# Kernel tuning notes

Measured on AMD Instinct MI355X. Metric: run time of the kernel, lower is better.

## Reference

```python
import jax, jax.numpy as jnp
import numpy as np

B, T, C = 64, 4096, 256
H = 4
HD = C // H  # head_dim = 64
EPS = 1e-5   # torch LayerNorm default


def setup_inputs() -> dict:
    key = jax.random.key(0)
    ks = jax.random.split(key, 8)
    x = jax.random.normal(ks[0], (B, T, C), dtype=jnp.float32)
    # per-head score MLP: Linear(C->HD) + Tanh + Linear(HD->1, no bias)
    W1 = jax.random.normal(ks[1], (H, C, HD), dtype=jnp.float32) * (1.0 / np.sqrt(C))
    b1 = jax.random.normal(ks[2], (H, HD), dtype=jnp.float32) * 0.02
    w2 = jax.random.normal(ks[3], (H, HD), dtype=jnp.float32) * (1.0 / np.sqrt(HD))
    # output projection Linear(H*C -> C), torch layout (out, in)
    Wo = jax.random.normal(ks[4], (C, H * C), dtype=jnp.float32) * (1.0 / np.sqrt(H * C))
    bo = jax.random.normal(ks[5], (C,), dtype=jnp.float32) * 0.02
    gamma = jnp.ones((C,), dtype=jnp.float32)
    beta = jnp.zeros((C,), dtype=jnp.float32)
    return {"x": x, "W1": W1, "b1": b1, "w2": w2, "Wo": Wo, "bo": bo,
            "gamma": gamma, "beta": beta}


def reference(x, W1, b1, w2, Wo, bo, gamma, beta):
    # All heads batched: hidden (B,H,T,HD)
    h = jnp.tanh(jnp.einsum('btc,hcd->bhtd', x, W1) + b1[None, :, None, :])
    scores = jnp.einsum('bhtd,hd->bht', h, w2)            # (B,H,T)
    weights = jax.nn.softmax(scores, axis=-1)             # softmax over T
    contexts = jnp.einsum('bht,btc->bhc', weights, x)     # (B,H,C)
    multi = contexts.reshape(B, H * C)                    # concat over heads
    out = multi @ Wo.T + bo                               # Linear(H*C->C)
    # LayerNorm over last dim (dropout is identity in eval mode)
    mu = jnp.mean(out, axis=-1, keepdims=True)
    var = jnp.mean(jnp.square(out - mu), axis=-1, keepdims=True)
    out = (out - mu) * jax.lax.rsqrt(var + EPS) * gamma + beta
    return out, weights
```

## Files before the change

kernel.cpp:

```cpp
#include <hip/hip_runtime.h>
#include <hip/hip_bf16.h>
#include <math.h>

#define B_ 64
#define T_ 4096
#define C_ 256
#define H_ 4
#define HD_ 64
#define EPS_ 1e-5f

typedef __attribute__((ext_vector_type(4))) float floatx4;
typedef __attribute__((ext_vector_type(8))) short short8;

#if __has_builtin(__builtin_amdgcn_cvt_pk_bf16_f32)
typedef __attribute__((ext_vector_type(2))) __bf16 bf16x2_t;
__device__ __forceinline__ unsigned int pack_bf16x2(float a, float b) {
    bf16x2_t v = __builtin_amdgcn_cvt_pk_bf16_f32(a, b);
    return __builtin_bit_cast(unsigned int, v);
}
#else
__device__ __forceinline__ unsigned int pack_bf16x2(float a, float b) {
    unsigned int ua = __builtin_bit_cast(unsigned int, a);
    unsigned int ub = __builtin_bit_cast(unsigned int, b);
    ua = (ua + 0x7fffu + ((ua >> 16) & 1u)) >> 16;
    ub = (ub + 0x7fffu + ((ub >> 16) & 1u)) >> 16;
    return ua | (ub << 16);
}
#endif

__device__ __forceinline__ float fast_tanh(float v) {
    float a = fabsf(v);
    float e = __expf(-2.0f * a);
    float r = (1.0f - e) / (1.0f + e);
    return copysignf(r, v);
}

__global__ void k0_w1t(const float* __restrict__ W1, unsigned short* __restrict__ w1t) {
    int n = blockIdx.x;
    int c = threadIdx.x;
    int h = n >> 6, d = n & 63;
    float v = W1[(h * C_ + c) * HD_ + d];
    unsigned int u = __builtin_bit_cast(unsigned int, v);
    u = (u + 0x7fffu + ((u >> 16) & 1u)) >> 16;
    w1t[n * C_ + c] = (unsigned short)u;
}

#define ASTRIDE 264
__global__ __launch_bounds__(256, 4)
void k1_fused(const float* __restrict__ x, const unsigned short* __restrict__ w1t,
              const float* __restrict__ b1, const float* __restrict__ w2,
              float* __restrict__ rawscore, float* __restrict__ ctxp,
              float* __restrict__ mS) {
    __shared__ __align__(16) unsigned short shA[64 * ASTRIDE];
    __shared__ float sS[4 * 64];
    __shared__ __align__(16) float sP4[64 * 4];

    const int tid  = threadIdx.x;
    const int lane = tid & 63;
    const int w    = tid >> 6;
    const int nl   = lane & 15;
    const int q    = lane >> 4;
    const int rowbase = blockIdx.x * 64;
    const int b       = blockIdx.x >> 6;
    const int tbase   = (blockIdx.x & 63) * 64;

    const int arow = tid >> 2;
    const int acol = (tid & 3) * 8;
    const float* aptr = x + (long)(rowbase + arow) * C_ + acol;
    #pragma unroll
    for (int kc = 0; kc < 8; ++kc) {
        const float4* ap = (const float4*)(aptr + kc * 32);
        float4 f0 = ap[0], f1 = ap[1];
        uint4 ua;
        ua.x = pack_bf16x2(f0.x, f0.y); ua.y = pack_bf16x2(f0.z, f0.w);
        ua.z = pack_bf16x2(f1.x, f1.y); ua.w = pack_bf16x2(f1.z, f1.w);
        *(uint4*)&shA[arow * ASTRIDE + kc * 32 + acol] = ua;
    }

    floatx4 acc[4][4];
    #pragma unroll
    for (int i = 0; i < 4; ++i)
        #pragma unroll
        for (int j = 0; j < 4; ++j)
            acc[i][j] = (floatx4){0.f, 0.f, 0.f, 0.f};

    const unsigned short* bBase = w1t + (long)(w * 64 + nl) * C_ + q * 8;
    __syncthreads();

    for (int ks = 0; ks < 8; ++ks) {
        uint4 bF[4];
        #pragma unroll
        for (int nb = 0; nb < 4; ++nb)
            bF[nb] = *(const uint4*)(bBase + nb * 16 * C_ + ks * 32);
        short8 aF[4];
        #pragma unroll
        for (int mb = 0; mb < 4; ++mb)
            aF[mb] = *(const short8*)&shA[(mb * 16 + nl) * ASTRIDE + ks * 32 + q * 8];
        #pragma unroll
        for (int mb = 0; mb < 4; ++mb)
            #pragma unroll
            for (int nb = 0; nb < 4; ++nb)
                acc[mb][nb] = __builtin_amdgcn_mfma_f32_16x16x32_bf16(
                    aF[mb], __builtin_bit_cast(short8, bF[nb]), acc[mb][nb], 0, 0, 0);
    }

    float b1v[4], w2v[4];
    #pragma unroll
    for (int nb = 0; nb < 4; ++nb) {
        int d = nb * 16 + nl;
        b1v[nb] = b1[w * HD_ + d];
        w2v[nb] = w2[w * HD_ + d];
    }
    #pragma unroll
    for (int mb = 0; mb < 4; ++mb) {
        float p[4];
        #pragma unroll
        for (int r = 0; r < 4; ++r) {
            float s = 0.f;
            #pragma unroll
            for (int nb = 0; nb < 4; ++nb)
                s += fast_tanh(acc[mb][nb][r] + b1v[nb]) * w2v[nb];
            p[r] = s;
        }
        #pragma unroll
        for (int m = 1; m < 16; m <<= 1)
            #pragma unroll
            for (int r = 0; r < 4; ++r)
                p[r] += __shfl_xor(p[r], m, 64);
        if (nl == 0) {
            #pragma unroll
            for (int r = 0; r < 4; ++r)
                sS[w * 64 + mb * 16 + q * 4 + r] = p[r];
        }
    }

    {
        float s = sS[w * 64 + lane];
        float m = s;
        #pragma unroll
        for (int off = 1; off < 64; off <<= 1)
            m = fmaxf(m, __shfl_xor(m, off, 64));
        float e = __expf(s - m);
        float Ss = e;
        #pragma unroll
        for (int off = 1; off < 64; off <<= 1)
            Ss += __shfl_xor(Ss, off, 64);
        sP4[lane * 4 + w] = e;
        rawscore[((long)(b * H_ + w)) * T_ + tbase + lane] = s;
        if (lane == 0) {
            mS[((long)blockIdx.x * H_ + w) * 2 + 0] = m;
            mS[((long)blockIdx.x * H_ + w) * 2 + 1] = Ss;
        }
    }
    __syncthreads();

    {
        float c0 = 0.f, c1 = 0.f, c2 = 0.f, c3 = 0.f;
        const float* xr = x + (long)rowbase * C_ + tid;
        const float4* pv4 = (const float4*)sP4;
        #pragma unroll 8
        for (int t = 0; t < 64; ++t) {
            float xv = xr[(long)t * C_];
            float4 pv = pv4[t];
            c0 += pv.x * xv;
            c1 += pv.y * xv;
            c2 += pv.z * xv;
            c3 += pv.w * xv;
        }
        float* o = ctxp + (long)blockIdx.x * (H_ * C_) + tid;
        o[0]   = c0;
        o[256] = c1;
        o[512] = c2;
        o[768] = c3;
    }
}

__global__ void k2_combine(const float* __restrict__ ctxp, const float* __restrict__ mS,
                           float* __restrict__ weights, float* __restrict__ multi) {
    __shared__ float sm[64], sSl[64], sc[64];
    int bh = blockIdx.x;
    int b = bh >> 2, h = bh & 3;
    int tid = threadIdx.x;
    if (tid < 64) {
        long blk = (long)b * 64 + tid;
        sm[tid]  = mS[(blk * H_ + h) * 2 + 0];
        sSl[tid] = mS[(blk * H_ + h) * 2 + 1];
    }
    __syncthreads();
    float m = -INFINITY;
    #pragma unroll 8
    for (int j = 0; j < 64; ++j) m = fmaxf(m, sm[j]);
    if (tid < 64) sc[tid] = __expf(sm[tid] - m);
    __syncthreads();
    float S = 0.f;
    #pragma unroll 8
    for (int j = 0; j < 64; ++j) S += sSl[j] * sc[j];
    float invS = 1.0f / S;

    float acc = 0.f;
    #pragma unroll 4
    for (int j = 0; j < 64; ++j)
        acc += ctxp[((long)(b * 64 + j) * H_ + h) * C_ + tid] * sc[j];
    multi[(long)b * (H_ * C_) + h * C_ + tid] = acc * invS;

    float* wr = weights + (long)bh * T_;
    #pragma unroll
    for (int i = 0; i < 16; ++i) {
        int t = tid + i * 256;
        float sv = wr[t];
        wr[t] = __expf(sv - m) * invS;
    }
}

__global__ void k4_out(const float* __restrict__ multiG, const float* __restrict__ Wo,
                       const float* __restrict__ bo, const float* __restrict__ gamma,
                       const float* __restrict__ beta, float* __restrict__ out) {
    __shared__ float multi[1024];
    __shared__ float red[256];
    int b = blockIdx.x, tid = threadIdx.x;
    {
        const float4* src = (const float4*)(multiG + (long)b * 1024);
        float4* dst = (float4*)multi;
        dst[tid] = src[tid];
    }
    __syncthreads();
    float a0 = 0.f, a1 = 0.f, a2 = 0.f, a3 = 0.f;
    const float4* wrow = (const float4*)(Wo + (long)tid * 1024);
    const float4* mv = (const float4*)multi;
    #pragma unroll 8
    for (int j4 = 0; j4 < 256; j4 += 4) {
        float4 w0 = wrow[j4],     m0 = mv[j4];
        float4 w1 = wrow[j4 + 1], m1 = mv[j4 + 1];
        float4 w2 = wrow[j4 + 2], m2 = mv[j4 + 2];
        float4 w3 = wrow[j4 + 3], m3 = mv[j4 + 3];
        a0 += m0.x * w0.x + m0.y * w0.y + m0.z * w0.z + m0.w * w0.w;
        a1 += m1.x * w1.x + m1.y * w1.y + m1.z * w1.z + m1.w * w1.w;
        a2 += m2.x * w2.x + m2.y * w2.y + m2.z * w2.z + m2.w * w2.w;
        a3 += m3.x * w3.x + m3.y * w3.y + m3.z * w3.z + m3.w * w3.w;
    }
    float acc = bo[tid] + ((a0 + a1) + (a2 + a3));
    red[tid] = acc; __syncthreads();
    for (int st = 128; st > 0; st >>= 1) {
        if (tid < st) red[tid] += red[tid + st];
        __syncthreads();
    }
    float mu = red[0] * (1.0f / 256.0f); __syncthreads();
    float dv = acc - mu;
    red[tid] = dv * dv; __syncthreads();
    for (int st = 128; st > 0; st >>= 1) {
        if (tid < st) red[tid] += red[tid + st];
        __syncthreads();
    }
    float var = red[0] * (1.0f / 256.0f);
    out[(long)b * C_ + tid] = dv * rsqrtf(var + EPS_) * gamma[tid] + beta[tid];
}

extern "C" void kernel_launch(void* const* d_in, const int* in_sizes, int n_in,
                              void* d_out, int out_size, void* d_ws, size_t ws_size,
                              hipStream_t stream) {
    const float* x     = (const float*)d_in[0];
    const float* W1    = (const float*)d_in[1];
    const float* b1    = (const float*)d_in[2];
    const float* w2    = (const float*)d_in[3];
    const float* Wo    = (const float*)d_in[4];
    const float* bo    = (const float*)d_in[5];
    const float* gamma = (const float*)d_in[6];
    const float* beta  = (const float*)d_in[7];

    float* out     = (float*)d_out;
    float* weights = out + B_ * C_;

    float* ctxp  = (float*)d_ws;
    float* mS    = ctxp + (long)4096 * H_ * C_;
    float* multi = mS + (long)4096 * H_ * 2;
    unsigned short* w1t = (unsigned short*)(multi + B_ * H_ * C_);

    k0_w1t    <<<256, 256, 0, stream>>>(W1, w1t);
    k1_fused  <<<4096, 256, 0, stream>>>(x, w1t, b1, w2, weights, ctxp, mS);
    k2_combine<<<256, 256, 0, stream>>>(ctxp, mS, weights, multi);
    k4_out    <<<64, 256, 0, stream>>>(multi, Wo, bo, gamma, beta, out);
}
```

Measured before the change: 475.9 us.

## Split fused score kernel across 512 threads and use fast reciprocal in tanh

New measurement: 545.0 us. 1.15x slower.

```diff
diff --git a/kernel.cpp b/kernel.cpp
--- a/kernel.cpp
+++ b/kernel.cpp
@@ -31,7 +31,11 @@
 __device__ __forceinline__ float fast_tanh(float v) {
     float a = fabsf(v);
     float e = __expf(-2.0f * a);
+#if __has_builtin(__builtin_amdgcn_rcpf)
+    float r = (1.0f - e) * __builtin_amdgcn_rcpf(1.0f + e);
+#else
     float r = (1.0f - e) / (1.0f + e);
+#endif
     return copysignf(r, v);
 }
 
@@ -46,7 +50,7 @@
 }
 
 #define ASTRIDE 264
-__global__ __launch_bounds__(256, 4)
+__global__ __launch_bounds__(512, 4)
 void k1_fused(const float* __restrict__ x, const unsigned short* __restrict__ w1t,
               const float* __restrict__ b1, const float* __restrict__ w2,
               float* __restrict__ rawscore, float* __restrict__ ctxp,
@@ -57,47 +61,51 @@
 
     const int tid  = threadIdx.x;
     const int lane = tid & 63;
-    const int w    = tid >> 6;
+    const int wid  = tid >> 6;
+    const int h    = wid >> 1;
+    const int mh   = wid & 1;
     const int nl   = lane & 15;
     const int q    = lane >> 4;
     const int rowbase = blockIdx.x * 64;
     const int b       = blockIdx.x >> 6;
     const int tbase   = (blockIdx.x & 63) * 64;
 
-    const int arow = tid >> 2;
-    const int acol = (tid & 3) * 8;
-    const float* aptr = x + (long)(rowbase + arow) * C_ + acol;
-    #pragma unroll
-    for (int kc = 0; kc < 8; ++kc) {
-        const float4* ap = (const float4*)(aptr + kc * 32);
-        float4 f0 = ap[0], f1 = ap[1];
-        uint4 ua;
-        ua.x = pack_bf16x2(f0.x, f0.y); ua.y = pack_bf16x2(f0.z, f0.w);
-        ua.z = pack_bf16x2(f1.x, f1.y); ua.w = pack_bf16x2(f1.z, f1.w);
-        *(uint4*)&shA[arow * ASTRIDE + kc * 32 + acol] = ua;
-    }
-
-    floatx4 acc[4][4];
-    #pragma unroll
-    for (int i = 0; i < 4; ++i)
+    {
+        const int arow = tid >> 3;
+        const int acol = (tid & 7) * 32;
+        const float4* ap = (const float4*)(x + (long)(rowbase + arow) * C_ + acol);
+        #pragma unroll
+        for (int i = 0; i < 4; ++i) {
+            float4 f0 = ap[2 * i], f1 = ap[2 * i + 1];
+            uint4 ua;
+            ua.x = pack_bf16x2(f0.x, f0.y); ua.y = pack_bf16x2(f0.z, f0.w);
+            ua.z = pack_bf16x2(f1.x, f1.y); ua.w = pack_bf16x2(f1.z, f1.w);
+            *(uint4*)&shA[arow * ASTRIDE + acol + i * 8] = ua;
+        }
+    }
+
+    floatx4 acc[2][4];
+    #pragma unroll
+    for (int i = 0; i < 2; ++i)
         #pragma unroll
         for (int j = 0; j < 4; ++j)
             acc[i][j] = (floatx4){0.f, 0.f, 0.f, 0.f};
 
-    const unsigned short* bBase = w1t + (long)(w * 64 + nl) * C_ + q * 8;
-    __syncthreads();
-
+    const unsigned short* bBase = w1t + (long)(h * 64 + nl) * C_ + q * 8;
+    __syncthreads();
+
+    #pragma unroll
     for (int ks = 0; ks < 8; ++ks) {
         uint4 bF[4];
         #pragma unroll
         for (int nb = 0; nb < 4; ++nb)
             bF[nb] = *(const uint4*)(bBase + nb * 16 * C_ + ks * 32);
-        short8 aF[4];
-        #pragma unroll
-        for (int mb = 0; mb < 4; ++mb)
-            aF[mb] = *(const short8*)&shA[(mb * 16 + nl) * ASTRIDE + ks * 32 + q * 8];
-        #pragma unroll
-        for (int mb = 0; mb < 4; ++mb)
+        short8 aF[2];
+        #pragma unroll
+        for (int mb = 0; mb < 2; ++mb)
+            aF[mb] = *(const short8*)&shA[(mh * 32 + mb * 16 + nl) * ASTRIDE + ks * 32 + q * 8];
+        #pragma unroll
+        for (int mb = 0; mb < 2; ++mb)
             #pragma unroll
             for (int nb = 0; nb < 4; ++nb)
                 acc[mb][nb] = __builtin_amdgcn_mfma_f32_16x16x32_bf16(
@@ -108,11 +116,11 @@
     #pragma unroll
     for (int nb = 0; nb < 4; ++nb) {
         int d = nb * 16 + nl;
-        b1v[nb] = b1[w * HD_ + d];
-        w2v[nb] = w2[w * HD_ + d];
-    }
-    #pragma unroll
-    for (int mb = 0; mb < 4; ++mb) {
+        b1v[nb] = b1[h * HD_ + d];
+        w2v[nb] = w2[h * HD_ + d];
+    }
+    #pragma unroll
+    for (int mb = 0; mb < 2; ++mb) {
         float p[4];
         #pragma unroll
         for (int r = 0; r < 4; ++r) {
@@ -130,11 +138,13 @@
         if (nl == 0) {
             #pragma unroll
             for (int r = 0; r < 4; ++r)
-                sS[w * 64 + mb * 16 + q * 4 + r] = p[r];
-        }
-    }
-
-    {
+                sS[h * 64 + mh * 32 + mb * 16 + q * 4 + r] = p[r];
+        }
+    }
+    __syncthreads();
+
+    if (tid < 256) {
+        const int w = tid >> 6;
         float s = sS[w * 64 + lane];
         float m = s;
         #pragma unroll
@@ -155,23 +165,21 @@
     __syncthreads();
 
     {
-        float c0 = 0.f, c1 = 0.f, c2 = 0.f, c3 = 0.f;
-        const float* xr = x + (long)rowbase * C_ + tid;
-        const float4* pv4 = (const float4*)sP4;
+        const int c  = tid & 255;
+        const int th = tid >> 8;
+        float c0 = 0.f, c1 = 0.f;
+        const float* xr = x + (long)rowbase * C_ + c;
+        const float2* pv2 = (const float2*)sP4;
         #pragma unroll 8
         for (int t = 0; t < 64; ++t) {
             float xv = xr[(long)t * C_];
-            float4 pv = pv4[t];
+            float2 pv = pv2[t * 2 + th];
             c0 += pv.x * xv;
             c1 += pv.y * xv;
-            c2 += pv.z * xv;
-            c3 += pv.w * xv;
-        }
-        float* o = ctxp + (long)blockIdx.x * (H_ * C_) + tid;
+        }
+        float* o = ctxp + (long)blockIdx.x * (H_ * C_) + th * 512 + c;
         o[0]   = c0;
         o[256] = c1;
-        o[512] = c2;
-        o[768] = c3;
     }
 }
 
@@ -276,7 +284,7 @@
     unsigned short* w1t = (unsigned short*)(multi + B_ * H_ * C_);
 
     k0_w1t    <<<256, 256, 0, stream>>>(W1, w1t);
-    k1_fused  <<<4096, 256, 0, stream>>>(x, w1t, b1, w2, weights, ctxp, mS);
+    k1_fused  <<<4096, 512, 0, stream>>>(x, w1t, b1, w2, weights, ctxp, mS);
     k2_combine<<<256, 256, 0, stream>>>(ctxp, mS, weights, multi);
     k4_out    <<<64, 256, 0, stream>>>(multi, Wo, bo, gamma, beta, out);
 }
```

## Pre-swizzle W1 into MFMA fragment order and double-buffer B-fragment loads

Applied to the files above, without the earlier changes.

Measured after the change: 467.2 us. About the same (-1.8%).

```diff
diff --git a/kernel.cpp b/kernel.cpp
--- a/kernel.cpp
+++ b/kernel.cpp
@@ -31,23 +31,34 @@
 __device__ __forceinline__ float fast_tanh(float v) {
     float a = fabsf(v);
     float e = __expf(-2.0f * a);
+#if __has_builtin(__builtin_amdgcn_rcpf)
+    float r = (1.0f - e) * __builtin_amdgcn_rcpf(1.0f + e);
+#else
     float r = (1.0f - e) / (1.0f + e);
+#endif
     return copysignf(r, v);
 }
 
-__global__ void k0_w1t(const float* __restrict__ W1, unsigned short* __restrict__ w1t) {
-    int n = blockIdx.x;
-    int c = threadIdx.x;
-    int h = n >> 6, d = n & 63;
-    float v = W1[(h * C_ + c) * HD_ + d];
-    unsigned int u = __builtin_bit_cast(unsigned int, v);
-    u = (u + 0x7fffu + ((u >> 16) & 1u)) >> 16;
-    w1t[n * C_ + c] = (unsigned short)u;
+__global__ void k0_w1frag(const float* __restrict__ W1, uint4* __restrict__ w1f) {
+    int h  = blockIdx.x >> 3;
+    int ks = blockIdx.x & 7;
+    int nb = threadIdx.x >> 6;
+    int l  = threadIdx.x & 63;
+    int nl = l & 15, q = l >> 4;
+    int d  = nb * 16 + nl;
+    const float* src = W1 + ((long)h * C_ + ks * 32 + q * 8) * HD_ + d;
+    float v[8];
+    #pragma unroll
+    for (int j = 0; j < 8; ++j) v[j] = src[j * HD_];
+    uint4 ua;
+    ua.x = pack_bf16x2(v[0], v[1]); ua.y = pack_bf16x2(v[2], v[3]);
+    ua.z = pack_bf16x2(v[4], v[5]); ua.w = pack_bf16x2(v[6], v[7]);
+    w1f[((long)blockIdx.x * 4 + nb) * 64 + l] = ua;
 }
 
 #define ASTRIDE 264
 __global__ __launch_bounds__(256, 4)
-void k1_fused(const float* __restrict__ x, const unsigned short* __restrict__ w1t,
+void k1_fused(const float* __restrict__ x, const uint4* __restrict__ w1f,
               const float* __restrict__ b1, const float* __restrict__ w2,
               float* __restrict__ rawscore, float* __restrict__ ctxp,
               float* __restrict__ mS) {
@@ -84,24 +95,39 @@
         for (int j = 0; j < 4; ++j)
             acc[i][j] = (floatx4){0.f, 0.f, 0.f, 0.f};
 
-    const unsigned short* bBase = w1t + (long)(w * 64 + nl) * C_ + q * 8;
-    __syncthreads();
-
-    for (int ks = 0; ks < 8; ++ks) {
-        uint4 bF[4];
-        #pragma unroll
-        for (int nb = 0; nb < 4; ++nb)
-            bF[nb] = *(const uint4*)(bBase + nb * 16 * C_ + ks * 32);
-        short8 aF[4];
-        #pragma unroll
-        for (int mb = 0; mb < 4; ++mb)
-            aF[mb] = *(const short8*)&shA[(mb * 16 + nl) * ASTRIDE + ks * 32 + q * 8];
-        #pragma unroll
-        for (int mb = 0; mb < 4; ++mb)
+    const uint4* bW = w1f + (long)w * (8 * 4 * 64) + lane;
+
+    uint4 bFa[4], bFb[4];
+    #pragma unroll
+    for (int nb = 0; nb < 4; ++nb) bFa[nb] = bW[nb * 64];
+
+    __syncthreads();
+
+    #pragma unroll
+    for (int kp = 0; kp < 4; ++kp) {
+        const int ks0 = 2 * kp, ks1 = 2 * kp + 1;
+        #pragma unroll
+        for (int nb = 0; nb < 4; ++nb) bFb[nb] = bW[(ks1 * 4 + nb) * 64];
+        #pragma unroll
+        for (int mb = 0; mb < 4; ++mb) {
+            short8 a = *(const short8*)&shA[(mb * 16 + nl) * ASTRIDE + ks0 * 32 + q * 8];
             #pragma unroll
             for (int nb = 0; nb < 4; ++nb)
                 acc[mb][nb] = __builtin_amdgcn_mfma_f32_16x16x32_bf16(
-                    aF[mb], __builtin_bit_cast(short8, bF[nb]), acc[mb][nb], 0, 0, 0);
+                    a, __builtin_bit_cast(short8, bFa[nb]), acc[mb][nb], 0, 0, 0);
+        }
+        if (kp < 3) {
+            #pragma unroll
+            for (int nb = 0; nb < 4; ++nb) bFa[nb] = bW[((ks0 + 2) * 4 + nb) * 64];
+        }
+        #pragma unroll
+        for (int mb = 0; mb < 4; ++mb) {
+            short8 a = *(const short8*)&shA[(mb * 16 + nl) * ASTRIDE + ks1 * 32 + q * 8];
+            #pragma unroll
+            for (int nb = 0; nb < 4; ++nb)
+                acc[mb][nb] = __builtin_amdgcn_mfma_f32_16x16x32_bf16(
+                    a, __builtin_bit_cast(short8, bFb[nb]), acc[mb][nb], 0, 0, 0);
+        }
     }
 
     float b1v[4], w2v[4];
@@ -273,10 +299,10 @@
     float* ctxp  = (float*)d_ws;
     float* mS    = ctxp + (long)4096 * H_ * C_;
     float* multi = mS + (long)4096 * H_ * 2;
-    unsigned short* w1t = (unsigned short*)(multi + B_ * H_ * C_);
-
-    k0_w1t    <<<256, 256, 0, stream>>>(W1, w1t);
-    k1_fused  <<<4096, 256, 0, stream>>>(x, w1t, b1, w2, weights, ctxp, mS);
+    uint4* w1f   = (uint4*)(multi + B_ * H_ * C_);
+
+    k0_w1frag <<<32, 256, 0, stream>>>(W1, w1f);
+    k1_fused  <<<4096, 256, 0, stream>>>(x, w1f, b1, w2, weights, ctxp, mS);
     k2_combine<<<256, 256, 0, stream>>>(ctxp, mS, weights, multi);
     k4_out    <<<64, 256, 0, stream>>>(multi, Wo, bo, gamma, beta, out);
 }
```
